# Kernel tuning notes

Hardware: AMD Instinct MI355X
Metric: run time of the kernel (lower is better)

Reference implementation:

```python
import jax, jax.numpy as jnp
import numpy as np
from jax import lax

B, L_IN, D, D_INNER = 4, 1024, 512, 512
H, DK = 8, 64
WIN = [4, 4, 4]
INNER_SIZE = 5   # temporal intra-level neighborhood size
SEM_K = 32       # opt.semantic_node: topk per level for semantic mask
N_LAYER = 2


def _build_temporal_mask(input_size, window_size, inner_size):
    # faithful port of Encoder.get_mask (Pyraformer-Naive mask)
    all_size = [input_size]
    for w in window_size:
        all_size.append(all_size[-1] // w)
    L = sum(all_size)
    m = np.zeros((L, L), dtype=np.float32)
    iw = inner_size // 2
    starts = [sum(all_size[:i]) for i in range(len(all_size))]
    for li, n in enumerate(all_size):
        st = starts[li]
        for i in range(st, st + n):
            m[i, max(i - iw, st):min(i + iw + 1, st + n)] = 1
    for li in range(1, len(all_size)):
        st = starts[li]
        prev = all_size[li - 1]
        w = window_size[li - 1]
        for i in range(st, st + all_size[li]):
            ls = st - prev + (i - st) * w
            rs = st if i == st + all_size[li] - 1 else st - prev + (i - st + 1) * w
            m[i, ls:rs] = 1
            m[ls:rs, i] = 1
    return (1 - m).astype(bool), all_size

TMASK_NP, ALL_SIZE = _build_temporal_mask(L_IN, WIN, INNER_SIZE)
L_TOT = sum(ALL_SIZE)  # 1360


def _ln(x, g, b, eps):
    mu = jnp.mean(x, axis=-1, keepdims=True)
    var = jnp.mean(jnp.square(x - mu), axis=-1, keepdims=True)
    return (x - mu) * lax.rsqrt(var + eps) * g + b


def _mha(x, Wq, Wk, Wv, fcW, fcb, g, b, mask):
    # post-norm MHA (normalize_before=False), dropout disabled (eval)
    Bq, L, _ = x.shape
    q = (x @ Wq).reshape(Bq, L, H, DK)
    k = (x @ Wk).reshape(Bq, L, H, DK)
    v = (x @ Wv).reshape(Bq, L, H, DK)
    a = jnp.einsum('bqhd,bkhd->bhqk', q, k) / np.float32(DK ** 0.5)
    a = jnp.where(mask, -jnp.inf, a)
    p = jax.nn.softmax(a, axis=-1)
    o = jnp.einsum('bhqk,bkhd->bqhd', p, v).reshape(Bq, L, H * DK)
    return _ln(o @ fcW + fcb + x, g, b, 1e-6)


def _semantic_mask(x):
    # get_semantic_mask: per-level cosine similarity, mask topk-most-similar within each level
    nrm = jnp.linalg.norm(x, axis=-1, keepdims=True)
    xn = x / jnp.maximum(nrm, 1e-8)
    sim = jnp.einsum('bid,bjd->bij', xn, xn)
    Bq = x.shape[0]
    mask = jnp.zeros((Bq, L_TOT, L_TOT), dtype=bool)
    bidx = jnp.arange(Bq)[:, None, None]
    start = 0
    for n in ALL_SIZE:
        k = min(n, SEM_K)
        blk = sim[:, start:start + n, start:start + n]
        idx = lax.top_k(blk, k)[1]              # [B, n, k]
        ridx = jnp.arange(n)[None, :, None]
        bm = jnp.zeros((Bq, n, n), dtype=bool).at[bidx, ridx, idx].set(True)
        mask = mask.at[:, start:start + n, start:start + n].set(bm)
        start += n
    return mask


def _bottleneck(x, dW, db, cW, cb, uW, ub, g, b):
    t = jnp.transpose(x @ dW + db, (0, 2, 1))  # [B, d_inner, L]
    outs = []
    for i in range(len(WIN)):
        t = lax.conv_general_dilated(t, cW[i], (WIN[i],), 'VALID',
                                     dimension_numbers=('NCH', 'OIH', 'NCH')) + cb[i][None, :, None]
        t = t / np.float32(np.sqrt(1.0 + 1e-5))  # eval BatchNorm with identity running stats
        t = jax.nn.elu(t)
        outs.append(t)
    pyr = jnp.transpose(jnp.concatenate(outs, axis=2), (0, 2, 1)) @ uW + ub
    return _ln(jnp.concatenate([x, pyr], axis=1), g, b, 1e-5)


def _forward(x_enc, down_W, down_b, conv_W, conv_b, up_W, up_b, bc_ln_g, bc_ln_b,
             attn_Wq, attn_Wk, attn_Wv, attn_fcW, attn_fcb, attn_ln_g, attn_ln_b,
             ffn_W1, ffn_b1, ffn_W2, ffn_b2, ffn_ln_g, ffn_ln_b):
    tmask = jnp.asarray(TMASK_NP)[None, None]  # [1,1,Lt,Lt]
    x = _bottleneck(x_enc, down_W, down_b, conv_W, conv_b, up_W, up_b, bc_ln_g, bc_ln_b)
    for l in range(N_LAYER):
        res = x
        t_out = _mha(x, attn_Wq[l, 0], attn_Wk[l, 0], attn_Wv[l, 0], attn_fcW[l, 0],
                     attn_fcb[l, 0], attn_ln_g[l, 0], attn_ln_b[l, 0], tmask)
        smask = _semantic_mask(x)[:, None]     # [B,1,Lt,Lt]
        s_out = _mha(x, attn_Wq[l, 1], attn_Wk[l, 1], attn_Wv[l, 1], attn_fcW[l, 1],
                     attn_fcb[l, 1], attn_ln_g[l, 1], attn_ln_b[l, 1], smask)
        x = (t_out + s_out + res) / 3.0
        res = x
        h = jax.nn.relu(x @ ffn_W1[l] + ffn_b1[l])
        x = _ln(h @ ffn_W2[l] + ffn_b2[l] + res, ffn_ln_g[l], ffn_ln_b[l], 1e-6)
    return x


def setup_inputs() -> dict:
    key = jax.random.key(0)
    ks = jax.random.split(key, 16)
    s = 0.02
    inp = {
        'x_enc': jax.random.normal(ks[0], (B, L_IN, D), jnp.float32),
        'down_W': jax.random.normal(ks[1], (D, D_INNER), jnp.float32) * s,
        'down_b': jnp.zeros((D_INNER,), jnp.float32),
        'conv_W': jax.random.normal(ks[2], (3, D_INNER, D_INNER, WIN[0]), jnp.float32) * s,
        'conv_b': jnp.zeros((3, D_INNER), jnp.float32),
        'up_W': jax.random.normal(ks[3], (D_INNER, D), jnp.float32) * s,
        'up_b': jnp.zeros((D,), jnp.float32),
        'bc_ln_g': jnp.ones((D,), jnp.float32),
        'bc_ln_b': jnp.zeros((D,), jnp.float32),
        'attn_Wq': jax.random.normal(ks[4], (N_LAYER, 2, D, H * DK), jnp.float32) * s,
        'attn_Wk': jax.random.normal(ks[5], (N_LAYER, 2, D, H * DK), jnp.float32) * s,
        'attn_Wv': jax.random.normal(ks[6], (N_LAYER, 2, D, H * DK), jnp.float32) * s,
        'attn_fcW': jax.random.normal(ks[7], (N_LAYER, 2, H * DK, D), jnp.float32) * s,
        'attn_fcb': jnp.zeros((N_LAYER, 2, D), jnp.float32),
        'attn_ln_g': jnp.ones((N_LAYER, 2, D), jnp.float32),
        'attn_ln_b': jnp.zeros((N_LAYER, 2, D), jnp.float32),
        'ffn_W1': jax.random.normal(ks[8], (N_LAYER, D, D_INNER), jnp.float32) * s,
        'ffn_b1': jnp.zeros((N_LAYER, D_INNER), jnp.float32),
        'ffn_W2': jax.random.normal(ks[9], (N_LAYER, D_INNER, D), jnp.float32) * s,
        'ffn_b2': jnp.zeros((N_LAYER, D), jnp.float32),
        'ffn_ln_g': jnp.ones((N_LAYER, D), jnp.float32),
        'ffn_ln_b': jnp.zeros((N_LAYER, D), jnp.float32),
    }
    return inp


def reference(x_enc, down_W, down_b, conv_W, conv_b, up_W, up_b, bc_ln_g, bc_ln_b,
              attn_Wq, attn_Wk, attn_Wv, attn_fcW, attn_fcb, attn_ln_g, attn_ln_b,
              ffn_W1, ffn_b1, ffn_W2, ffn_b2, ffn_ln_g, ffn_ln_b):
    return _forward(x_enc, down_W, down_b, conv_W, conv_b, up_W, up_b, bc_ln_g, bc_ln_b,
                    attn_Wq, attn_Wk, attn_Wv, attn_fcW, attn_fcb, attn_ln_g, attn_ln_b,
                    ffn_W1, ffn_b1, ffn_W2, ffn_b2, ffn_ln_g, ffn_ln_b)
```

## Files before the change

### kernel.cpp

```cpp
#include <hip/hip_runtime.h>
#include <float.h>
#include <math.h>
#include <stdint.h>

#define LT 1360
#define BB 4
#define DM 512
#define NHH 8
#define NBLE 2785280
#define MBW 24
#define QSCALE 0.18033688f

typedef __attribute__((ext_vector_type(8))) short short8;
typedef __attribute__((ext_vector_type(4))) float f32x4;
typedef unsigned long long u64;

__device__ __forceinline__ ushort f2b(float x){
    uint32_t u = __float_as_uint(x);
    return (ushort)((u + 0x7fffu + ((u >> 16) & 1u)) >> 16);
}
__device__ __forceinline__ float b2f(ushort u){
    return __uint_as_float(((uint32_t)u) << 16);
}
__device__ __forceinline__ float ex2(float x){
    float r;
    asm("v_exp_f32 %0, %1" : "=v"(r) : "v"(x));
    return r;
}
__device__ __forceinline__ uint32_t pkbf(float lo, float hi){
    uint32_t r;
    asm("v_cvt_pk_bf16_f32 %0, %1, %2" : "=v"(r) : "v"(lo), "v"(hi));
    return r;
}

#define SG0 0
#define SG1 1048576
#define SG2 (SG1 + 65536)
#define SG3 (SG2 + 4096)
#define SBT (SG3 + 256)

__device__ __forceinline__ void blk_info(int i, int& bi, int& st, int& n){
    if (i < 1024){ bi = 0; st = 0;    n = 1024; }
    else if (i < 1280){ bi = 1; st = 1024; n = 256; }
    else if (i < 1344){ bi = 2; st = 1280; n = 64; }
    else { bi = 3; st = 1344; n = 16; }
}

__global__ __launch_bounds__(256)
void build_tidx(int* __restrict__ idx, int* __restrict__ cnt){
    int i = blockIdx.x * 256 + threadIdx.x;
    if (i >= LT) return;
    int bi, st, n; blk_info(i, bi, st, n);
    int c = 0; int* row = idx + i * 12;
    int lo = (i - 2 > st) ? i - 2 : st;
    int hi = (i + 2 < st + n - 1) ? i + 2 : st + n - 1;
    for (int j = lo; j <= hi; j++) row[c++] = j;
    if (bi < 3) row[c++] = st + n + (i - st) / 4;
    if (bi > 0){
        int stc = st - n * 4;
        int base = stc + (i - st) * 4;
        for (int t = 0; t < 4; t++) row[c++] = base + t;
    }
    cnt[i] = c;
    for (int t = c; t < 12; t++) row[t] = 0;
}

__global__ __launch_bounds__(256)
void wtrans(const float* __restrict__ W, ushort* __restrict__ Wt, int K, int N, long dstStride){
    int mat = blockIdx.z;
    const float* Ws = W + (size_t)mat * K * N;
    ushort* Wd = Wt + (size_t)mat * dstStride;
    int k0 = blockIdx.y << 6, n0 = blockIdx.x << 6;
    __shared__ ushort t[64][72];
    int tid = threadIdx.x;
    #pragma unroll
    for (int p = 0; p < 4; p++){
        int idx = tid + (p << 8);
        int r = idx >> 4, c4 = (idx & 15) << 2;
        float4 v = *(const float4*)(Ws + (size_t)(k0 + r) * N + n0 + c4);
        t[c4+0][r] = f2b(v.x); t[c4+1][r] = f2b(v.y);
        t[c4+2][r] = f2b(v.z); t[c4+3][r] = f2b(v.w);
    }
    __syncthreads();
    #pragma unroll
    for (int p = 0; p < 4; p++){
        int idx = tid + (p << 8);
        int r = idx >> 4, c4 = (idx & 15) << 2;
        *(uint2*)&Wd[(size_t)(n0 + r) * K + k0 + c4] = *(uint2*)&t[r][c4];
    }
}

__global__ __launch_bounds__(256)
void wconv(const float* __restrict__ cw, ushort* __restrict__ wt){
    int conv = blockIdx.y;
    const float* src = cw + (size_t)conv * 512 * 512 * 4;
    ushort* dst = wt + (size_t)conv * 2048 * 512;
    int idx = blockIdx.x * 256 + threadIdx.x;
    int o = idx >> 11, rest = idx & 2047;
    int k = rest >> 9, ii = rest & 511;
    dst[idx] = f2b(src[((size_t)(o << 9) + ii) * 4 + k]);
}

__global__ __launch_bounds__(256)
void gemm_qkv(const ushort* __restrict__ A, const ushort* __restrict__ Bw,
              void* __restrict__ Cout, int M, int N, int K)
{
    __shared__ ushort As[64][72];
    __shared__ ushort Bs[128][72];
    int tid = threadIdx.x;
    int lane = tid & 63, w = tid >> 6, quad = lane >> 4, l15 = lane & 15;
    int gm = blockIdx.y << 6, gn = blockIdx.x << 7;
    int arow = tid >> 2, ac = (tid & 3) << 4;
    int brow = tid >> 1, bc = (tid & 1) << 5;
    f32x4 acc[4][2];
    #pragma unroll
    for (int mi = 0; mi < 4; mi++)
        #pragma unroll
        for (int ni = 0; ni < 2; ni++)
            acc[mi][ni] = (f32x4){0.f,0.f,0.f,0.f};
    const ushort* Ap = A + (size_t)(gm + arow) * K + ac;
    const ushort* Bp = Bw + (size_t)(gn + brow) * K + bc;
    uint4 a0r = *(const uint4*)(Ap);
    uint4 a1r = *(const uint4*)(Ap + 8);
    uint4 b0r = *(const uint4*)(Bp);
    uint4 b1r = *(const uint4*)(Bp + 8);
    uint4 b2r = *(const uint4*)(Bp + 16);
    uint4 b3r = *(const uint4*)(Bp + 24);
    *(uint4*)&As[arow][ac]     = a0r;  *(uint4*)&As[arow][ac + 8]  = a1r;
    *(uint4*)&Bs[brow][bc]     = b0r;  *(uint4*)&Bs[brow][bc + 8]  = b1r;
    *(uint4*)&Bs[brow][bc + 16] = b2r; *(uint4*)&Bs[brow][bc + 24] = b3r;
    __syncthreads();
    for (int k0 = 0; k0 < K; k0 += 64){
        bool nx = (k0 + 64 < K);
        if (nx){
            a0r = *(const uint4*)(Ap + k0 + 64);
            a1r = *(const uint4*)(Ap + k0 + 72);
            b0r = *(const uint4*)(Bp + k0 + 64);
            b1r = *(const uint4*)(Bp + k0 + 72);
            b2r = *(const uint4*)(Bp + k0 + 80);
            b3r = *(const uint4*)(Bp + k0 + 88);
        }
        __builtin_amdgcn_s_setprio(1);
        #pragma unroll
        for (int kk = 0; kk < 2; kk++){
            short8 af[4], bf[2];
            #pragma unroll
            for (int mi = 0; mi < 4; mi++)
                af[mi] = *(const short8*)&As[(mi << 4) + l15][(kk << 5) + (quad << 3)];
            #pragma unroll
            for (int ni = 0; ni < 2; ni++)
                bf[ni] = *(const short8*)&Bs[(w << 5) + (ni << 4) + l15][(kk << 5) + (quad << 3)];
            #pragma unroll
            for (int mi = 0; mi < 4; mi++)
                #pragma unroll
                for (int ni = 0; ni < 2; ni++)
                    acc[mi][ni] = __builtin_amdgcn_mfma_f32_16x16x32_bf16(af[mi], bf[ni], acc[mi][ni], 0, 0, 0);
        }
        __builtin_amdgcn_s_setprio(0);
        if (nx){
            __syncthreads();
            *(uint4*)&As[arow][ac]     = a0r;  *(uint4*)&As[arow][ac + 8]  = a1r;
            *(uint4*)&Bs[brow][bc]     = b0r;  *(uint4*)&Bs[brow][bc + 8]  = b1r;
            *(uint4*)&Bs[brow][bc + 16] = b2r; *(uint4*)&Bs[brow][bc + 24] = b3r;
            __syncthreads();
        }
    }
    int seg = gn >> 9, gc = gn & 511;
    ushort* Ob = (ushort*)Cout;
    if (seg == 0){
        #pragma unroll
        for (int mi = 0; mi < 4; mi++)
            #pragma unroll
            for (int r = 0; r < 4; r++){
                int row = gm + (mi << 4) + (quad << 2) + r;
                #pragma unroll
                for (int ni = 0; ni < 2; ni++){
                    int c5 = gc + (w << 5) + (ni << 4) + l15;
                    Ob[(size_t)row * 512 + c5] = f2b(acc[mi][ni][r] * QSCALE);
                }
            }
    } else if (seg == 1){
        #pragma unroll
        for (int mi = 0; mi < 4; mi++)
            #pragma unroll
            for (int r = 0; r < 4; r++){
                int row = gm + (mi << 4) + (quad << 2) + r;
                #pragma unroll
                for (int ni = 0; ni < 2; ni++){
                    int c5 = gc + (w << 5) + (ni << 4) + l15;
                    Ob[(size_t)2*NBLE + (size_t)row * 512 + c5] = f2b(acc[mi][ni][r]);
                }
            }
    } else {
        __syncthreads();
        #pragma unroll
        for (int mi = 0; mi < 4; mi++)
            #pragma unroll
            for (int r = 0; r < 4; r++){
                int rloc = (mi << 4) + (quad << 2) + r;
                int row = gm + rloc;
                #pragma unroll
                for (int ni = 0; ni < 2; ni++){
                    int cloc = (w << 5) + (ni << 4) + l15;
                    ushort hv = f2b(acc[mi][ni][r]);
                    Ob[(size_t)5*NBLE + (size_t)row * 512 + gc + cloc] = hv;
                    Bs[cloc][rloc] = hv;
                }
            }
        __syncthreads();
        int colw = tid >> 3;
        int jo = (tid & 7) << 3;
        int rr = gm + jo;
        int bb = rr / LT;
        int ii = rr - bb * LT;
        #pragma unroll
        for (int cc = 0; cc < 4; cc++){
            int c = colw + (cc << 5);
            uint4 tv = *(const uint4*)&Bs[c][jo];
            ushort* dst = Ob + (size_t)4*NBLE + ((size_t)(bb * 512 + gc + c)) * LT + ii;
            *(uint4*)dst = tv;
        }
    }
}

template<int ABF>
__global__ __launch_bounds__(256)
void gemm64t(const void* __restrict__ Avp, const ushort* __restrict__ Bw,
             const float* __restrict__ bias, const float* __restrict__ Rres,
             void* __restrict__ Cout, int M, int N, int K,
             int act, int omode, int mpb, int orpb, int ooff)
{
    __shared__ ushort As[64][72];
    __shared__ ushort Bs[64][72];
    int tid = threadIdx.x;
    int lane = tid & 63, w = tid >> 6, quad = lane >> 4, l15 = lane & 15;
    int gm = blockIdx.y << 6, gn = blockIdx.x << 6;
    int wr = (w >> 1) << 5, wc = (w & 1) << 5;
    int srow = tid >> 2, sc = (tid & 3) << 4;
    f32x4 acc[2][2];
    #pragma unroll
    for (int mi = 0; mi < 2; mi++)
        #pragma unroll
        for (int ni = 0; ni < 2; ni++)
            acc[mi][ni] = (f32x4){0.f,0.f,0.f,0.f};
    const float*  Af = (const float*)Avp;
    const ushort* Ab = (const ushort*)Avp;
    size_t aoff = (size_t)(gm + srow) * K + sc;
    const ushort* Bp = Bw + (size_t)(gn + srow) * K + sc;
    uint4 aR0, aR1, bR0, bR1;
    float4 f0, f1, f2v, f3v;
    if (ABF){
        aR0 = *(const uint4*)(Ab + aoff);
        aR1 = *(const uint4*)(Ab + aoff + 8);
    } else {
        f0  = *(const float4*)(Af + aoff);
        f1  = *(const float4*)(Af + aoff + 4);
        f2v = *(const float4*)(Af + aoff + 8);
        f3v = *(const float4*)(Af + aoff + 12);
    }
    bR0 = *(const uint4*)(Bp);
    bR1 = *(const uint4*)(Bp + 8);
    if (!ABF){
        aR0.x = (uint32_t)f2b(f0.x)  | ((uint32_t)f2b(f0.y)  << 16);
        aR0.y = (uint32_t)f2b(f0.z)  | ((uint32_t)f2b(f0.w)  << 16);
        aR0.z = (uint32_t)f2b(f1.x)  | ((uint32_t)f2b(f1.y)  << 16);
        aR0.w = (uint32_t)f2b(f1.z)  | ((uint32_t)f2b(f1.w)  << 16);
        aR1.x = (uint32_t)f2b(f2v.x) | ((uint32_t)f2b(f2v.y) << 16);
        aR1.y = (uint32_t)f2b(f2v.z) | ((uint32_t)f2b(f2v.w) << 16);
        aR1.z = (uint32_t)f2b(f3v.x) | ((uint32_t)f2b(f3v.y) << 16);
        aR1.w = (uint32_t)f2b(f3v.z) | ((uint32_t)f2b(f3v.w) << 16);
    }
    *(uint4*)&As[srow][sc]     = aR0;
    *(uint4*)&As[srow][sc + 8] = aR1;
    *(uint4*)&Bs[srow][sc]     = bR0;
    *(uint4*)&Bs[srow][sc + 8] = bR1;
    __syncthreads();
    for (int k0 = 0; k0 < K; k0 += 64){
        bool nx = (k0 + 64 < K);
        if (nx){
            if (ABF){
                aR0 = *(const uint4*)(Ab + aoff + k0 + 64);
                aR1 = *(const uint4*)(Ab + aoff + k0 + 72);
            } else {
                f0  = *(const float4*)(Af + aoff + k0 + 64);
                f1  = *(const float4*)(Af + aoff + k0 + 68);
                f2v = *(const float4*)(Af + aoff + k0 + 72);
                f3v = *(const float4*)(Af + aoff + k0 + 76);
            }
            bR0 = *(const uint4*)(Bp + k0 + 64);
            bR1 = *(const uint4*)(Bp + k0 + 72);
        }
        __builtin_amdgcn_s_setprio(1);
        #pragma unroll
        for (int kk = 0; kk < 2; kk++){
            short8 af0 = *(const short8*)&As[wr + l15][(kk << 5) + (quad << 3)];
            short8 af1 = *(const short8*)&As[wr + 16 + l15][(kk << 5) + (quad << 3)];
            short8 bf0 = *(const short8*)&Bs[wc + l15][(kk << 5) + (quad << 3)];
            short8 bf1 = *(const short8*)&Bs[wc + 16 + l15][(kk << 5) + (quad << 3)];
            acc[0][0] = __builtin_amdgcn_mfma_f32_16x16x32_bf16(af0, bf0, acc[0][0], 0, 0, 0);
            acc[0][1] = __builtin_amdgcn_mfma_f32_16x16x32_bf16(af0, bf1, acc[0][1], 0, 0, 0);
            acc[1][0] = __builtin_amdgcn_mfma_f32_16x16x32_bf16(af1, bf0, acc[1][0], 0, 0, 0);
            acc[1][1] = __builtin_amdgcn_mfma_f32_16x16x32_bf16(af1, bf1, acc[1][1], 0, 0, 0);
        }
        __builtin_amdgcn_s_setprio(0);
        if (nx){
            __syncthreads();
            if (!ABF){
                aR0.x = (uint32_t)f2b(f0.x)  | ((uint32_t)f2b(f0.y)  << 16);
                aR0.y = (uint32_t)f2b(f0.z)  | ((uint32_t)f2b(f0.w)  << 16);
                aR0.z = (uint32_t)f2b(f1.x)  | ((uint32_t)f2b(f1.y)  << 16);
                aR0.w = (uint32_t)f2b(f1.z)  | ((uint32_t)f2b(f1.w)  << 16);
                aR1.x = (uint32_t)f2b(f2v.x) | ((uint32_t)f2b(f2v.y) << 16);
                aR1.y = (uint32_t)f2b(f2v.z) | ((uint32_t)f2b(f2v.w) << 16);
                aR1.z = (uint32_t)f2b(f3v.x) | ((uint32_t)f2b(f3v.y) << 16);
                aR1.w = (uint32_t)f2b(f3v.z) | ((uint32_t)f2b(f3v.w) << 16);
            }
            *(uint4*)&As[srow][sc]     = aR0;
            *(uint4*)&As[srow][sc + 8] = aR1;
            *(uint4*)&Bs[srow][sc]     = bR0;
            *(uint4*)&Bs[srow][sc + 8] = bR1;
            __syncthreads();
        }
    }
    #pragma unroll
    for (int mi = 0; mi < 2; mi++){
        #pragma unroll
        for (int r = 0; r < 4; r++){
            int row = gm + wr + (mi << 4) + (quad << 2) + r;
            #pragma unroll
            for (int ni = 0; ni < 2; ni++){
                int col = gn + wc + (ni << 4) + l15;
                float v = acc[mi][ni][r];
                if (bias) v += bias[col];
                if (Rres) v += Rres[(size_t)row * N + col];
                if (act == 2){ v = fmaxf(v, 0.f); }
                if (omode == 0){
                    int orow = mpb ? (row / mpb) * orpb + ooff + (row % mpb) : row;
                    ((float*)Cout)[(size_t)orow * N + col] = v;
                } else {
                    ((ushort*)Cout)[(size_t)row * N + col] = f2b(v);
                }
            }
        }
    }
}

__global__ __launch_bounds__(256)
void gemm_sk(const float* __restrict__ A, const ushort* __restrict__ Bw,
             float* __restrict__ P, int M, int N, int K, int kslice)
{
    __shared__ ushort As[64][40];
    __shared__ ushort Bs[64][40];
    int tid = threadIdx.x;
    int lane = tid & 63, w = tid >> 6, quad = lane >> 4, l15 = lane & 15;
    int gm = blockIdx.y << 6, gn = blockIdx.x << 6;
    int wr = (w >> 1) << 5, wc = (w & 1) << 5;
    int srow = tid >> 2, sc8 = (tid & 3) << 3;
    int ks = blockIdx.z * kslice;
    f32x4 acc[2][2];
    #pragma unroll
    for (int mi = 0; mi < 2; mi++)
        #pragma unroll
        for (int ni = 0; ni < 2; ni++)
            acc[mi][ni] = (f32x4){0.f,0.f,0.f,0.f};
    const float* Ap = A + (size_t)(gm + srow) * K;
    const ushort* Bp = Bw + (size_t)(gn + srow) * K;
    for (int k0 = ks; k0 < ks + kslice; k0 += 32){
        float4 a0 = *(const float4*)(Ap + k0 + sc8);
        float4 a1 = *(const float4*)(Ap + k0 + sc8 + 4);
        uint4 av;
        av.x = (uint32_t)f2b(a0.x) | ((uint32_t)f2b(a0.y) << 16);
        av.y = (uint32_t)f2b(a0.z) | ((uint32_t)f2b(a0.w) << 16);
        av.z = (uint32_t)f2b(a1.x) | ((uint32_t)f2b(a1.y) << 16);
        av.w = (uint32_t)f2b(a1.z) | ((uint32_t)f2b(a1.w) << 16);
        *(uint4*)&As[srow][sc8] = av;
        *(uint4*)&Bs[srow][sc8] = *(const uint4*)(Bp + k0 + sc8);
        __syncthreads();
        short8 af0 = *(const short8*)&As[wr + l15][quad << 3];
        short8 af1 = *(const short8*)&As[wr + 16 + l15][quad << 3];
        short8 bf0 = *(const short8*)&Bs[wc + l15][quad << 3];
        short8 bf1 = *(const short8*)&Bs[wc + 16 + l15][quad << 3];
        acc[0][0] = __builtin_amdgcn_mfma_f32_16x16x32_bf16(af0, bf0, acc[0][0], 0, 0, 0);
        acc[0][1] = __builtin_amdgcn_mfma_f32_16x16x32_bf16(af0, bf1, acc[0][1], 0, 0, 0);
        acc[1][0] = __builtin_amdgcn_mfma_f32_16x16x32_bf16(af1, bf0, acc[1][0], 0, 0, 0);
        acc[1][1] = __builtin_amdgcn_mfma_f32_16x16x32_bf16(af1, bf1, acc[1][1], 0, 0, 0);
        __syncthreads();
    }
    float* Pz = P + (size_t)blockIdx.z * M * N;
    #pragma unroll
    for (int mi = 0; mi < 2; mi++){
        #pragma unroll
        for (int r = 0; r < 4; r++){
            int row = gm + wr + (mi << 4) + (quad << 2) + r;
            #pragma unroll
            for (int ni = 0; ni < 2; ni++){
                int col = gn + wc + (ni << 4) + l15;
                Pz[(size_t)row * N + col] = acc[mi][ni][r];
            }
        }
    }
}

__global__ __launch_bounds__(256)
void sk_reduce(const float* __restrict__ P, const float* __restrict__ bias,
               float* __restrict__ C, int MN, int S)
{
    int idx = (blockIdx.x * 256 + threadIdx.x) << 2;
    if (idx >= MN) return;
    float4 s = {0.f, 0.f, 0.f, 0.f};
    for (int z = 0; z < S; z++){
        float4 v = *(const float4*)(P + (size_t)z * MN + idx);
        s.x += v.x; s.y += v.y; s.z += v.z; s.w += v.w;
    }
    const float cscale = 0.9999950000375f;
    int col = idx & 511;
    float o[4] = {s.x, s.y, s.z, s.w};
    #pragma unroll
    for (int t = 0; t < 4; t++){
        float v = (o[t] + bias[col + t]) * cscale;
        o[t] = (v > 0.f) ? v : expm1f(v);
    }
    *(float4*)(C + idx) = (float4){o[0], o[1], o[2], o[3]};
}

__global__ __launch_bounds__(256)
void sim_mfma(const ushort* __restrict__ XH, const ushort* __restrict__ XL,
              float* __restrict__ SIM){
    __shared__ ushort Ah[64][40], Al[64][40], Bh[64][40], Bl[64][40];
    int x = blockIdx.x, b = blockIdx.y;
    int ti, tj, st, n, goff;
    if (x < 256){ ti = x >> 4; tj = x & 15; st = 0; n = 1024; goff = SG0; }
    else if (x < 272){ int y = x - 256; ti = y >> 2; tj = y & 3; st = 1024; n = 256; goff = SG1; }
    else if (x == 272){ ti = 0; tj = 0; st = 1280; n = 64; goff = SG2; }
    else { ti = 0; tj = 0; st = 1344; n = 16; goff = SG3; }
    const ushort* XbH = XH + (((size_t)b * LT + st) << 9);
    const ushort* XbL = XL + (((size_t)b * LT + st) << 9);
    float* Cb = SIM + (size_t)b * SBT + goff;
    int gm = ti << 6, gn = tj << 6;
    int tid = threadIdx.x;
    int lane = tid & 63, w = tid >> 6, quad = lane >> 4, l15 = lane & 15;
    int wr = (w >> 1) << 5, wc = (w & 1) << 5;
    int srow = tid >> 2, sc8 = (tid & 3) << 3;
    int ra = gm + srow; if (ra > n - 1) ra = n - 1;
    int rb = gn + srow; if (rb > n - 1) rb = n - 1;
    f32x4 acc[2][2];
    #pragma unroll
    for (int mi = 0; mi < 2; mi++)
        #pragma unroll
        for (int ni = 0; ni < 2; ni++)
            acc[mi][ni] = (f32x4){0.f,0.f,0.f,0.f};
    for (int k0 = 0; k0 < 512; k0 += 32){
        *(uint4*)&Ah[srow][sc8] = *(const uint4*)(XbH + ((size_t)ra << 9) + k0 + sc8);
        *(uint4*)&Al[srow][sc8] = *(const uint4*)(XbL + ((size_t)ra << 9) + k0 + sc8);
        *(uint4*)&Bh[srow][sc8] = *(const uint4*)(XbH + ((size_t)rb << 9) + k0 + sc8);
        *(uint4*)&Bl[srow][sc8] = *(const uint4*)(XbL + ((size_t)rb << 9) + k0 + sc8);
        __syncthreads();
        short8 ah0 = *(const short8*)&Ah[wr + l15][quad << 3];
        short8 ah1 = *(const short8*)&Ah[wr + 16 + l15][quad << 3];
        short8 al0 = *(const short8*)&Al[wr + l15][quad << 3];
        short8 al1 = *(const short8*)&Al[wr + 16 + l15][quad << 3];
        short8 bh0 = *(const short8*)&Bh[wc + l15][quad << 3];
        short8 bh1 = *(const short8*)&Bh[wc + 16 + l15][quad << 3];
        short8 bl0 = *(const short8*)&Bl[wc + l15][quad << 3];
        short8 bl1 = *(const short8*)&Bl[wc + 16 + l15][quad << 3];
        acc[0][0] = __builtin_amdgcn_mfma_f32_16x16x32_bf16(ah0, bh0, acc[0][0], 0, 0, 0);
        acc[0][0] = __builtin_amdgcn_mfma_f32_16x16x32_bf16(ah0, bl0, acc[0][0], 0, 0, 0);
        acc[0][0] = __builtin_amdgcn_mfma_f32_16x16x32_bf16(al0, bh0, acc[0][0], 0, 0, 0);
        acc[0][1] = __builtin_amdgcn_mfma_f32_16x16x32_bf16(ah0, bh1, acc[0][1], 0, 0, 0);
        acc[0][1] = __builtin_amdgcn_mfma_f32_16x16x32_bf16(ah0, bl1, acc[0][1], 0, 0, 0);
        acc[0][1] = __builtin_amdgcn_mfma_f32_16x16x32_bf16(al0, bh1, acc[0][1], 0, 0, 0);
        acc[1][0] = __builtin_amdgcn_mfma_f32_16x16x32_bf16(ah1, bh0, acc[1][0], 0, 0, 0);
        acc[1][0] = __builtin_amdgcn_mfma_f32_16x16x32_bf16(ah1, bl0, acc[1][0], 0, 0, 0);
        acc[1][0] = __builtin_amdgcn_mfma_f32_16x16x32_bf16(al1, bh0, acc[1][0], 0, 0, 0);
        acc[1][1] = __builtin_amdgcn_mfma_f32_16x16x32_bf16(ah1, bh1, acc[1][1], 0, 0, 0);
        acc[1][1] = __builtin_amdgcn_mfma_f32_16x16x32_bf16(ah1, bl1, acc[1][1], 0, 0, 0);
        acc[1][1] = __builtin_amdgcn_mfma_f32_16x16x32_bf16(al1, bh1, acc[1][1], 0, 0, 0);
        __syncthreads();
    }
    #pragma unroll
    for (int mi = 0; mi < 2; mi++){
        #pragma unroll
        for (int r = 0; r < 4; r++){
            int row = gm + wr + (mi << 4) + (quad << 2) + r;
            if (row < n){
                #pragma unroll
                for (int ni = 0; ni < 2; ni++){
                    int col = gn + wc + (ni << 4) + l15;
                    if (col < n) Cb[(size_t)row * n + col] = acc[mi][ni][r];
                }
            }
        }
    }
}

__global__ __launch_bounds__(256)
void pcat_copy(const float* __restrict__ C1, const float* __restrict__ C2,
               const float* __restrict__ C3, float* __restrict__ PC){
    int idx = blockIdx.x * 256 + threadIdx.x;
    int d = idx & 511;
    int r = (idx >> 9) % 336;
    int b = idx / (336 * 512);
    float v;
    if (r < 256)       v = C1[(((size_t)b * 256 + r) << 9) + d];
    else if (r < 320)  v = C2[(((size_t)b * 64 + (r - 256)) << 9) + d];
    else               v = C3[(((size_t)b * 16 + (r - 320)) << 9) + d];
    PC[idx] = v;
}

__global__ __launch_bounds__(256)
void xenc_copy(const float* __restrict__ xe, float* __restrict__ dst){
    int idx = blockIdx.x * 256 + threadIdx.x;
    int d = idx & 511;
    int l = (idx >> 9) & 1023;
    int b = idx >> 19;
    dst[(((size_t)b * LT + l) << 9) + d] = xe[idx];
}

__global__ __launch_bounds__(256)
void ln_kernel(const float* __restrict__ in, const float* __restrict__ g,
               const float* __restrict__ bta, float* __restrict__ out,
               ushort* __restrict__ ob, float eps){
    int wid = threadIdx.x >> 6, lane = threadIdx.x & 63;
    int row = blockIdx.x * 4 + wid;
    const float* p = in + ((size_t)row << 9);
    float vals[8]; float s = 0.f, s2 = 0.f;
    #pragma unroll
    for (int t = 0; t < 8; t++){
        float v = p[lane + t * 64]; vals[t] = v; s += v; s2 += v * v;
    }
    #pragma unroll
    for (int off = 32; off; off >>= 1){
        s  += __shfl_xor(s,  off, 64);
        s2 += __shfl_xor(s2, off, 64);
    }
    float mu = s * (1.f / 512.f);
    float var = s2 * (1.f / 512.f) - mu * mu;
    float r = rsqrtf(var + eps);
    float* q = out + ((size_t)row << 9);
    ushort* qb = ob ? ob + ((size_t)row << 9) : nullptr;
    #pragma unroll
    for (int t = 0; t < 8; t++){
        int c = lane + t * 64;
        float v = (vals[t] - mu) * r * g[c] + bta[c];
        q[c] = v;
        if (qb) qb[c] = f2b(v);
    }
}

__global__ __launch_bounds__(256)
void ln_add3(const float* __restrict__ in, const float* __restrict__ g,
             const float* __restrict__ bta, const float* __restrict__ T,
             float* __restrict__ X, ushort* __restrict__ ob, float eps){
    int wid = threadIdx.x >> 6, lane = threadIdx.x & 63;
    int row = blockIdx.x * 4 + wid;
    const float* p = in + ((size_t)row << 9);
    float vals[8]; float s = 0.f, s2 = 0.f;
    #pragma unroll
    for (int t = 0; t < 8; t++){
        float v = p[lane + t * 64]; vals[t] = v; s += v; s2 += v * v;
    }
    #pragma unroll
    for (int off = 32; off; off >>= 1){
        s  += __shfl_xor(s,  off, 64);
        s2 += __shfl_xor(s2, off, 64);
    }
    float mu = s * (1.f / 512.f);
    float var = s2 * (1.f / 512.f) - mu * mu;
    float r = rsqrtf(var + eps);
    const float* tp = T + ((size_t)row << 9);
    float* xp = X + ((size_t)row << 9);
    ushort* qb = ob + ((size_t)row << 9);
    #pragma unroll
    for (int t = 0; t < 8; t++){
        int c = lane + t * 64;
        float sn = (vals[t] - mu) * r * g[c] + bta[c];
        float nv = (tp[c] + sn + xp[c]) * (1.f / 3.f);
        xp[c] = nv;
        qb[c] = f2b(nv);
    }
}

__global__ __launch_bounds__(256)
void rownorm_kernel(const float* __restrict__ in, ushort* __restrict__ XHp,
                    ushort* __restrict__ XLp){
    int wid = threadIdx.x >> 6, lane = threadIdx.x & 63;
    int row = blockIdx.x * 4 + wid;
    const float* p = in + ((size_t)row << 9);
    float vals[8]; float s2 = 0.f;
    #pragma unroll
    for (int t = 0; t < 8; t++){
        float v = p[lane + t * 64]; vals[t] = v; s2 += v * v;
    }
    #pragma unroll
    for (int off = 32; off; off >>= 1) s2 += __shfl_xor(s2, off, 64);
    float inv = 1.f / fmaxf(sqrtf(s2), 1e-8f);
    ushort* qh = XHp + ((size_t)row << 9);
    ushort* ql = XLp + ((size_t)row << 9);
    #pragma unroll
    for (int t = 0; t < 8; t++){
        float v = vals[t] * inv;
        ushort h = f2b(v);
        qh[lane + t * 64] = h;
        ql[lane + t * 64] = f2b(v - b2f(h));
    }
}

__global__ __launch_bounds__(256)
void topk_sel(const float* __restrict__ SIM, u64* __restrict__ MB){
    int wid = threadIdx.x >> 6, lane = threadIdx.x & 63;
    int r = blockIdx.x * 4 + wid;
    int b = r / LT, i = r % LT;
    int bi, st, n; blk_info(i, bi, st, n);
    u64* mrow = MB + ((size_t)b * LT + i) * MBW;
    if (n == 16){
        u64 myw = 0;
        if (lane == 21) myw = ~0ULL;
        if (lane < MBW) mrow[lane] = myw;
        return;
    }
    int goff = (bi == 0) ? SG0 : (bi == 1) ? SG1 : SG2;
    const float* srow = SIM + (size_t)b * SBT + goff + (size_t)(i - st) * n;
    int ns = n >> 6;
    float vals[16];
    #pragma unroll
    for (int t = 0; t < 16; t++)
        vals[t] = (t < ns) ? srow[lane + (t << 6)] : -FLT_MAX;

    float c[32];
    #pragma unroll
    for (int t = 0; t < 16; t++) c[t] = vals[t];
    #pragma unroll
    for (int k = 2; k <= 16; k <<= 1){
        #pragma unroll
        for (int j = k >> 1; j > 0; j >>= 1){
            #pragma unroll
            for (int t = 0; t < 16; t++){
                int l = t ^ j;
                if (l > t){
                    float lo = fminf(c[t], c[l]);
                    float hi = fmaxf(c[t], c[l]);
                    if ((t & k) == 0){ c[t] = hi; c[l] = lo; }
                    else             { c[t] = lo; c[l] = hi; }
                }
            }
        }
    }
    #pragma unroll
    for (int t = 16; t < 32; t++) c[t] = -FLT_MAX;

    float V32;
    #pragma unroll
    for (int rd = 0; rd < 6; rd++){
        float f[32];
        #pragma unroll
        for (int t = 0; t < 32; t++) f[t] = __shfl_xor(c[t], 1 << rd, 64);
        float m[32];
        #pragma unroll
        for (int t = 0; t < 32; t++) m[t] = fmaxf(c[t], f[31 - t]);
        if (rd < 5){
            #pragma unroll
            for (int d = 16; d >= 1; d >>= 1){
                #pragma unroll
                for (int t = 0; t < 32; t++){
                    if ((t & d) == 0){
                        float lo = fminf(m[t], m[t + d]);
                        m[t] = fmaxf(m[t], m[t + d]);
                        m[t + d] = lo;
                    }
                }
            }
            #pragma unroll
            for (int t = 0; t < 32; t++) c[t] = m[t];
        } else {
            float mn = m[0];
            #pragma unroll
            for (int t = 1; t < 32; t++) mn = fminf(mn, m[t]);
            V32 = mn;
        }
    }

    int cnt_gt = 0;
    #pragma unroll
    for (int t = 0; t < 16; t++){
        u64 bg = __ballot(vals[t] > V32);
        cnt_gt += __popcll(bg);
    }
    int need = 32 - cnt_gt;
    u64 lmask = (1ULL << lane) - 1;
    u64 myw = 0;
    if (lane == 21) myw = 0xFFFFFFFFFFFF0000ULL;
    int eqrun = 0;
    int w0 = st >> 6;
    #pragma unroll
    for (int t = 0; t < 16; t++){
        bool eq = (vals[t] == V32);
        u64 beq = __ballot(eq);
        int below = __popcll(beq & lmask);
        bool sel = (vals[t] > V32) || (eq && (eqrun + below) < need);
        eqrun += __popcll(beq);
        u64 wsel = __ballot(sel);
        if (t < ns && lane == w0 + t) myw = wsel;
    }
    if (lane < MBW) mrow[lane] = myw;
}

__global__ __launch_bounds__(256)
void attn_sparse(const ushort* __restrict__ Q, const ushort* __restrict__ Kp,
                 const ushort* __restrict__ Vn, const int* __restrict__ IDX,
                 const int* __restrict__ CNT, ushort* __restrict__ O){
    int wid = threadIdx.x >> 6, lane = threadIdx.x & 63;
    int row = blockIdx.x * 4 + wid;
    int b = row / (NHH * LT);
    int rem = row % (NHH * LT);
    int h = rem / LT, i = rem % LT;
    int c = CNT[i];
    int jl = IDX[i * 12 + (lane % 12)];
    float qd = b2f(Q[(((size_t)b * LT + i) << 9) + h * 64 + lane]);
    const ushort* kb = Kp + (((size_t)b * LT) << 9) + h * 64 + lane;
    const ushort* vb = Vn + (((size_t)b * LT) << 9) + h * 64 + lane;
    int jj[12];
    #pragma unroll
    for (int t = 0; t < 12; t++) jj[t] = __shfl(jl, t, 64);
    float kv[12], vv[12];
    #pragma unroll
    for (int t = 0; t < 12; t++){
        kv[t] = b2f(kb[(size_t)jj[t] << 9]);
        vv[t] = b2f(vb[(size_t)jj[t] << 9]);
    }
    float lsum = 0.f, o = 0.f;
    #pragma unroll
    for (int t = 0; t < 12; t++){
        float s = qd * kv[t];
        #pragma unroll
        for (int off = 32; off; off >>= 1) s += __shfl_xor(s, off, 64);
        float p = (t < c) ? exp2f(s) : 0.f;
        lsum += p;
        o += p * vv[t];
    }
    O[(((size_t)b * LT + i) << 9) + h * 64 + lane] = f2b(o / lsum);
}

__global__ __launch_bounds__(256)
void flash_mfma(const ushort* __restrict__ Q, const ushort* __restrict__ Kp,
                const ushort* __restrict__ Vt, const u64* __restrict__ MB,
                float* __restrict__ FO0, float* __restrict__ FO1,
                float* __restrict__ LP)
{
    __shared__ ushort Ks[64][76];
    __shared__ ushort Vs[64][76];
    __shared__ ushort Ps[4][16][76];
    int bh = blockIdx.x, b = bh >> 3, h = bh & 7;
    int q0 = blockIdx.y << 6;
    int half = blockIdx.z;
    int tid = threadIdx.x;
    int w = tid >> 6, lane = tid & 63, quad = lane >> 4, l15 = lane & 15;

    int qm = q0 + w * 16 + l15;
    int qmc = (qm < LT) ? qm : (LT - 1);
    const ushort* qp = Q + ((size_t)(b * LT + qmc) << 9) + h * 64 + (quad << 3);
    short8 qf0 = *(const short8*)qp;
    short8 qf1 = *(const short8*)(qp + 32);

    float l_acc[4] = {0.f, 0.f, 0.f, 0.f};
    f32x4 Oacc[4];
    #pragma unroll
    for (int dt = 0; dt < 4; dt++) Oacc[dt] = (f32x4){0.f,0.f,0.f,0.f};

    int srow = tid >> 2, sc = (tid & 3) << 4;
    int ktS = half * 11, ktE = ktS + 11;

    const ushort* kpp = Kp + ((size_t)(b * LT + (ktS << 6) + srow) << 9) + h * 64 + sc;
    const ushort* vpp = Vt + (size_t)(b * 512 + h * 64 + srow) * LT + (ktS << 6) + sc;
    int mr0 = q0 + (w << 4) + (quad << 2);
    const u64* mpp = MB + ((size_t)b * LT + mr0) * MBW + ktS;

    {
        uint4 k0v = *(const uint4*)kpp;
        uint4 k1v = *(const uint4*)(kpp + 8);
        uint4 v0v = *(const uint4*)vpp;
        uint4 v1v = *(const uint4*)(vpp + 8);
        kpp += 64 * 512; vpp += 64;
        *(uint4*)&Ks[srow][sc]     = k0v;
        *(uint4*)&Ks[srow][sc + 8] = k1v;
        *(uint4*)&Vs[srow][sc]     = v0v;
        *(uint4*)&Vs[srow][sc + 8] = v1v;
    }
    __syncthreads();

    for (int kt = ktS; kt < ktE; kt++){
        bool havenext = (kt + 1 < ktE);
        uint4 kn0, kn1, vn0, vn1;
        if (havenext){
            kn0 = *(const uint4*)kpp;
            kn1 = *(const uint4*)(kpp + 8);
            vn0 = *(const uint4*)vpp;
            vn1 = *(const uint4*)(vpp + 8);
            kpp += 64 * 512; vpp += 64;
        }
        u64 mb0 = mpp[0], mb1 = mpp[MBW], mb2 = mpp[2 * MBW], mb3 = mpp[3 * MBW];
        mpp++;
        f32x4 s[4];
        #pragma unroll
        for (int nt = 0; nt < 4; nt++) s[nt] = (f32x4){0.f,0.f,0.f,0.f};
        __builtin_amdgcn_s_setprio(1);
        #pragma unroll
        for (int nt = 0; nt < 4; nt++){
            short8 kf0 = *(const short8*)&Ks[(nt << 4) + l15][quad << 3];
            short8 kf1 = *(const short8*)&Ks[(nt << 4) + l15][32 + (quad << 3)];
            s[nt] = __builtin_amdgcn_mfma_f32_16x16x32_bf16(qf0, kf0, s[nt], 0, 0, 0);
            s[nt] = __builtin_amdgcn_mfma_f32_16x16x32_bf16(qf1, kf1, s[nt], 0, 0, 0);
        }
        __builtin_amdgcn_s_setprio(0);
        u64 mbs[4] = {mb0, mb1, mb2, mb3};
        #pragma unroll
        for (int r = 0; r < 4; r++){
            u64 sh = mbs[r] >> l15;
            uint32_t blo = (uint32_t)sh, bhi = (uint32_t)(sh >> 32);
            float p0 = (blo & 1u)         ? 0.f : ex2(s[0][r]);
            float p1 = ((blo >> 16) & 1u) ? 0.f : ex2(s[1][r]);
            float p2 = (bhi & 1u)         ? 0.f : ex2(s[2][r]);
            float p3 = ((bhi >> 16) & 1u) ? 0.f : ex2(s[3][r]);
            uint32_t pk01 = pkbf(p0, p1);
            uint32_t pk23 = pkbf(p2, p3);
            int prow = (quad << 2) + r;
            Ps[w][prow][l15]      = (ushort)pk01;
            Ps[w][prow][16 + l15] = (ushort)(pk01 >> 16);
            Ps[w][prow][32 + l15] = (ushort)pk23;
            Ps[w][prow][48 + l15] = (ushort)(pk23 >> 16);
            l_acc[r] += (p0 + p1) + (p2 + p3);
        }
        short8 pf0 = *(const short8*)&Ps[w][l15][quad << 3];
        short8 pf1 = *(const short8*)&Ps[w][l15][32 + (quad << 3)];
        __builtin_amdgcn_s_setprio(1);
        #pragma unroll
        for (int dt = 0; dt < 4; dt++){
            short8 vf0 = *(const short8*)&Vs[(dt << 4) + l15][quad << 3];
            short8 vf1 = *(const short8*)&Vs[(dt << 4) + l15][32 + (quad << 3)];
            Oacc[dt] = __builtin_amdgcn_mfma_f32_16x16x32_bf16(pf0, vf0, Oacc[dt], 0, 0, 0);
            Oacc[dt] = __builtin_amdgcn_mfma_f32_16x16x32_bf16(pf1, vf1, Oacc[dt], 0, 0, 0);
        }
        __builtin_amdgcn_s_setprio(0);
        if (havenext){
            __syncthreads();
            *(uint4*)&Ks[srow][sc]     = kn0;
            *(uint4*)&Ks[srow][sc + 8] = kn1;
            *(uint4*)&Vs[srow][sc]     = vn0;
            *(uint4*)&Vs[srow][sc + 8] = vn1;
            __syncthreads();
        }
    }
    #pragma unroll
    for (int r = 0; r < 4; r++){
        #pragma unroll
        for (int off = 1; off < 16; off <<= 1)
            l_acc[r] += __shfl_xor(l_acc[r], off, 64);
    }
    float* FO = half ? FO1 : FO0;
    float* Lp = LP + (size_t)half * BB * NHH * LT;
    #pragma unroll
    for (int r = 0; r < 4; r++){
        int qrow = q0 + (w << 4) + (quad << 2) + r;
        if (qrow < LT){
            #pragma unroll
            for (int dt = 0; dt < 4; dt++)
                FO[((size_t)(b * LT + qrow) << 9) + h * 64 + (dt << 4) + l15] = Oacc[dt][r];
            if (l15 == 0)
                Lp[(size_t)(b * NHH + h) * LT + qrow] = l_acc[r];
        }
    }
}

__global__ __launch_bounds__(256)
void flash_combine(const float* __restrict__ FO0, const float* __restrict__ FO1,
                   const float* __restrict__ LP, ushort* __restrict__ AO){
    int wid = threadIdx.x >> 6, lane = threadIdx.x & 63;
    int row = blockIdx.x * 4 + wid;
    int b = row / LT, q = row % LT;
    size_t base = (size_t)row << 9;
    const float* Lp0 = LP;
    const float* Lp1 = LP + (size_t)BB * NHH * LT;
    #pragma unroll
    for (int t = 0; t < 8; t++){
        size_t li = (size_t)(b * NHH + t) * LT + q;
        float inv = 1.f / (Lp0[li] + Lp1[li]);
        int c = lane + t * 64;
        AO[base + c] = f2b((FO0[base + c] + FO1[base + c]) * inv);
    }
}

extern "C" void kernel_launch(void* const* d_in, const int* in_sizes, int n_in,
                              void* d_out, int out_size, void* d_ws, size_t ws_size,
                              hipStream_t stream)
{
    const float* x_enc   = (const float*)d_in[0];
    const float* down_W  = (const float*)d_in[1];
    const float* down_b  = (const float*)d_in[2];
    const float* conv_W  = (const float*)d_in[3];
    const float* conv_b  = (const float*)d_in[4];
    const float* up_W    = (const float*)d_in[5];
    const float* up_b    = (const float*)d_in[6];
    const float* bc_g    = (const float*)d_in[7];
    const float* bc_b    = (const float*)d_in[8];
    const float* aWq     = (const float*)d_in[9];
    const float* aWk     = (const float*)d_in[10];
    const float* aWv     = (const float*)d_in[11];
    const float* afcW    = (const float*)d_in[12];
    const float* afcb    = (const float*)d_in[13];
    const float* alng    = (const float*)d_in[14];
    const float* alnb    = (const float*)d_in[15];
    const float* fW1     = (const float*)d_in[16];
    const float* fb1     = (const float*)d_in[17];
    const float* fW2     = (const float*)d_in[18];
    const float* fb2     = (const float*)d_in[19];
    const float* flng    = (const float*)d_in[20];
    const float* flnb    = (const float*)d_in[21];

    const size_t NBL = (size_t)NBLE;
    float* X   = (float*)d_ws;
    float* TMP = X   + NBL;
    float* Qb  = TMP + NBL;
    float* Kb  = Qb  + NBL;
    float* Vb  = Kb  + NBL;
    float* AO  = Vb  + NBL;
    float* TO  = AO  + NBL;
    float* SO  = TO  + NBL;
    u64* MBm = (u64*)(SO + NBL);
    int* TIDX = (int*)(MBm + (size_t)BB * LT * MBW);
    int* TCNT = TIDX + (size_t)LT * 12;
    ushort* WG = (ushort*)(TCNT + LT);
    const size_t M512 = 262144;
    ushort* WdownT = WG;                 size_t wo = M512;
    ushort* WupT   = WG + wo;            wo += M512;
    ushort* Wqkv   = WG + wo;            wo += 12 * M512;
    ushort* WfT    = WG + wo;            wo += 4 * M512;
    ushort* W1T    = WG + wo;            wo += 2 * M512;
    ushort* W2T    = WG + wo;            wo += 2 * M512;
    ushort* WCt    = WG + wo;            wo += 3 * 1048576;
    float* LP = (float*)(WG + wo);
    size_t need = 8 * NBL * sizeof(float) + (size_t)BB * LT * MBW * 8
                + (size_t)LT * 13 * 4 + wo * sizeof(ushort)
                + (size_t)2 * BB * NHH * LT * 4;
    if (ws_size < need) return;

    float* Y    = Qb;
    float* C1   = Kb;
    float* C2   = C1 + (size_t)BB*256*512;
    float* C3   = C2 + (size_t)BB*64*512;
    float* PCAT = Vb;
    float* SKP  = AO;
    ushort* XNh = (ushort*)AO;
    ushort* XNl = XNh + NBLE;
    float* SIMB = Qb;
    ushort* QbH = (ushort*)Qb;
    ushort* KbH = (ushort*)Kb;
    ushort* VtH = (ushort*)Vb;
    ushort* VnH = VtH + NBLE;
    float* FO0  = TMP;
    float* FO1  = SO;
    ushort* XB  = (ushort*)SO;
    ushort* AOb = (ushort*)AO;
    ushort* HfB = (ushort*)Qb;

    auto gemmN = [&](const void* A, int abf, const ushort* Bw, const float* bias,
                     const float* res, void* C, int M,
                     int act, int omode, int mpb, int orpb, int ooff){
        dim3 grid(8, M / 64);
        if (abf) gemm64t<1><<<grid, 256, 0, stream>>>(A, Bw, bias, res, C, M, 512, 512,
                                                      act, omode, mpb, orpb, ooff);
        else     gemm64t<0><<<grid, 256, 0, stream>>>(A, Bw, bias, res, C, M, 512, 512,
                                                      act, omode, mpb, orpb, ooff);
    };
    auto convG = [&](const float* A, const ushort* Bw, const float* bias,
                     float* C, int M){
        const int S = 8, K = 2048, N = 512;
        gemm_sk<<<dim3(8, M / 64, S), 256, 0, stream>>>(A, Bw, SKP, M, N, K, K / S);
        sk_reduce<<<(M * N) / 1024, 256, 0, stream>>>(SKP, bias, C, M * N, S);
    };

    build_tidx<<<(LT + 255) / 256, 256, 0, stream>>>(TIDX, TCNT);
    wtrans<<<dim3(8, 8, 1), 256, 0, stream>>>(down_W, WdownT, 512, 512, M512);
    wtrans<<<dim3(8, 8, 1), 256, 0, stream>>>(up_W,   WupT,   512, 512, M512);
    wtrans<<<dim3(8, 8, 4), 256, 0, stream>>>(aWq,  Wqkv + 0 * M512, 512, 512, 3 * (long)M512);
    wtrans<<<dim3(8, 8, 4), 256, 0, stream>>>(aWk,  Wqkv + 1 * M512, 512, 512, 3 * (long)M512);
    wtrans<<<dim3(8, 8, 4), 256, 0, stream>>>(aWv,  Wqkv + 2 * M512, 512, 512, 3 * (long)M512);
    wtrans<<<dim3(8, 8, 4), 256, 0, stream>>>(afcW, WfT, 512, 512, M512);
    wtrans<<<dim3(8, 8, 2), 256, 0, stream>>>(fW1,  W1T, 512, 512, M512);
    wtrans<<<dim3(8, 8, 2), 256, 0, stream>>>(fW2,  W2T, 512, 512, M512);
    wconv<<<dim3(4096, 3), 256, 0, stream>>>(conv_W, WCt);

    gemmN(x_enc, 0, WdownT, down_b, nullptr, Y, BB*1024, 0, 0, 0, 0, 0);
    convG(Y,  WCt,             conv_b + 0,    C1, BB*256);
    convG(C1, WCt + 1048576,   conv_b + 512,  C2, BB*64);
    convG(C2, WCt + 2*1048576, conv_b + 1024, C3, BB*16);
    pcat_copy<<<(BB*336*512)/256, 256, 0, stream>>>(C1, C2, C3, PCAT);
    gemmN(PCAT, 0, WupT, up_b, nullptr, TMP, BB*336, 0, 0, 336, LT, 1024);
    xenc_copy<<<(BB*1024*512)/256, 256, 0, stream>>>(x_enc, TMP);
    ln_kernel<<<(BB*LT)/4, 256, 0, stream>>>(TMP, bc_g, bc_b, X, XB, 1e-5f);

    for (int l = 0; l < 2; l++){
        rownorm_kernel<<<(BB*LT)/4, 256, 0, stream>>>(X, XNh, XNl);
        sim_mfma<<<dim3(274, BB), 256, 0, stream>>>(XNh, XNl, SIMB);
        topk_sel<<<(BB*LT)/4, 256, 0, stream>>>(SIMB, MBm);

        for (int j = 0; j < 2; j++){
            int li = l * 2 + j;
            const float* bf = afcb + (size_t)li * 512;
            const float* lg = alng + (size_t)li * 512;
            const float* lb = alnb + (size_t)li * 512;
            gemm_qkv<<<dim3(12, 85), 256, 0, stream>>>(XB, Wqkv + (size_t)li * 3 * M512,
                                                       QbH, BB*LT, 1536, 512);
            if (j == 0){
                attn_sparse<<<(BB*NHH*LT)/4, 256, 0, stream>>>(QbH, KbH, VnH, TIDX, TCNT, AOb);
            } else {
                flash_mfma<<<dim3(32, 22, 2), 256, 0, stream>>>(QbH, KbH, VtH, MBm, FO0, FO1, LP);
                flash_combine<<<(BB*LT)/4, 256, 0, stream>>>(FO0, FO1, LP, AOb);
            }
            gemmN(AOb, 1, WfT + (size_t)li * M512, bf, X, TMP, BB*LT, 0, 0, 0, 0, 0);
            if (j == 0)
                ln_kernel<<<(BB*LT)/4, 256, 0, stream>>>(TMP, lg, lb, TO, nullptr, 1e-6f);
            else
                ln_add3<<<(BB*LT)/4, 256, 0, stream>>>(TMP, lg, lb, TO, X, XB, 1e-6f);
        }

        gemmN(XB,  1, W1T + (size_t)l * M512, fb1 + (size_t)l*512, nullptr, HfB, BB*LT, 2, 1, 0, 0, 0);
        gemmN(HfB, 1, W2T + (size_t)l * M512, fb2 + (size_t)l*512, X, TMP, BB*LT, 0, 0, 0, 0, 0);
        ln_kernel<<<(BB*LT)/4, 256, 0, stream>>>(TMP, flng + (size_t)l*512, flnb + (size_t)l*512,
                                                 (l == 1) ? (float*)d_out : X,
                                                 (l == 1) ? nullptr : XB, 1e-6f);
    }
}
```

Baseline: 821.5 us.

## Drop split-K flash attention and combine kernel; double-buffer K/V tiles in LDS

The flash attention kernel no longer splits the 22 key tiles across two blocks. One block now covers all keys, normalizes by the softmax sum and writes bf16 output directly, so the float partial outputs and the separate combine kernel go away. K/V tiles are double-buffered in shared memory, which cuts the two barriers per iteration to one. The trade-off is half as many blocks (704), which lowers parallelism on a large GPU, and more LDS per block.

```diff
diff --git a/kernel.cpp b/kernel.cpp
--- a/kernel.cpp
+++ b/kernel.cpp
@@ -743,15 +743,13 @@
 __global__ __launch_bounds__(256)
 void flash_mfma(const ushort* __restrict__ Q, const ushort* __restrict__ Kp,
                 const ushort* __restrict__ Vt, const u64* __restrict__ MB,
-                float* __restrict__ FO0, float* __restrict__ FO1,
-                float* __restrict__ LP)
+                ushort* __restrict__ AO)
 {
-    __shared__ ushort Ks[64][76];
-    __shared__ ushort Vs[64][76];
+    __shared__ ushort Ks[2][64][76];
+    __shared__ ushort Vs[2][64][76];
     __shared__ ushort Ps[4][16][76];
     int bh = blockIdx.x, b = bh >> 3, h = bh & 7;
     int q0 = blockIdx.y << 6;
-    int half = blockIdx.z;
     int tid = threadIdx.x;
     int w = tid >> 6, lane = tid & 63, quad = lane >> 4, l15 = lane & 15;
 
@@ -767,12 +765,11 @@
     for (int dt = 0; dt < 4; dt++) Oacc[dt] = (f32x4){0.f,0.f,0.f,0.f};
 
     int srow = tid >> 2, sc = (tid & 3) << 4;
-    int ktS = half * 11, ktE = ktS + 11;
-
-    const ushort* kpp = Kp + ((size_t)(b * LT + (ktS << 6) + srow) << 9) + h * 64 + sc;
-    const ushort* vpp = Vt + (size_t)(b * 512 + h * 64 + srow) * LT + (ktS << 6) + sc;
+
+    const ushort* kpp = Kp + ((size_t)(b * LT + srow) << 9) + h * 64 + sc;
+    const ushort* vpp = Vt + (size_t)(b * 512 + h * 64 + srow) * LT + sc;
     int mr0 = q0 + (w << 4) + (quad << 2);
-    const u64* mpp = MB + ((size_t)b * LT + mr0) * MBW + ktS;
+    const u64* mpp = MB + ((size_t)b * LT + mr0) * MBW;
 
     {
         uint4 k0v = *(const uint4*)kpp;
@@ -780,15 +777,16 @@
         uint4 v0v = *(const uint4*)vpp;
         uint4 v1v = *(const uint4*)(vpp + 8);
         kpp += 64 * 512; vpp += 64;
-        *(uint4*)&Ks[srow][sc]     = k0v;
-        *(uint4*)&Ks[srow][sc + 8] = k1v;
-        *(uint4*)&Vs[srow][sc]     = v0v;
-        *(uint4*)&Vs[srow][sc + 8] = v1v;
+        *(uint4*)&Ks[0][srow][sc]     = k0v;
+        *(uint4*)&Ks[0][srow][sc + 8] = k1v;
+        *(uint4*)&Vs[0][srow][sc]     = v0v;
+        *(uint4*)&Vs[0][srow][sc + 8] = v1v;
     }
     __syncthreads();
 
-    for (int kt = ktS; kt < ktE; kt++){
-        bool havenext = (kt + 1 < ktE);
+    for (int kt = 0; kt < 22; kt++){
+        int cur = kt & 1;
+        bool havenext = (kt + 1 < 22);
         uint4 kn0, kn1, vn0, vn1;
         if (havenext){
             kn0 = *(const uint4*)kpp;
@@ -805,8 +803,8 @@
         __builtin_amdgcn_s_setprio(1);
         #pragma unroll
         for (int nt = 0; nt < 4; nt++){
-            short8 kf0 = *(const short8*)&Ks[(nt << 4) + l15][quad << 3];
-            short8 kf1 = *(const short8*)&Ks[(nt << 4) + l15][32 + (quad << 3)];
+            short8 kf0 = *(const short8*)&Ks[cur][(nt << 4) + l15][quad << 3];
+            short8 kf1 = *(const short8*)&Ks[cur][(nt << 4) + l15][32 + (quad << 3)];
             s[nt] = __builtin_amdgcn_mfma_f32_16x16x32_bf16(qf0, kf0, s[nt], 0, 0, 0);
             s[nt] = __builtin_amdgcn_mfma_f32_16x16x32_bf16(qf1, kf1, s[nt], 0, 0, 0);
         }
@@ -834,20 +832,20 @@
         __builtin_amdgcn_s_setprio(1);
         #pragma unroll
         for (int dt = 0; dt < 4; dt++){
-            short8 vf0 = *(const short8*)&Vs[(dt << 4) + l15][quad << 3];
-            short8 vf1 = *(const short8*)&Vs[(dt << 4) + l15][32 + (quad << 3)];
+            short8 vf0 = *(const short8*)&Vs[cur][(dt << 4) + l15][quad << 3];
+            short8 vf1 = *(const short8*)&Vs[cur][(dt << 4) + l15][32 + (quad << 3)];
             Oacc[dt] = __builtin_amdgcn_mfma_f32_16x16x32_bf16(pf0, vf0, Oacc[dt], 0, 0, 0);
             Oacc[dt] = __builtin_amdgcn_mfma_f32_16x16x32_bf16(pf1, vf1, Oacc[dt], 0, 0, 0);
         }
         __builtin_amdgcn_s_setprio(0);
         if (havenext){
-            __syncthreads();
-            *(uint4*)&Ks[srow][sc]     = kn0;
-            *(uint4*)&Ks[srow][sc + 8] = kn1;
-            *(uint4*)&Vs[srow][sc]     = vn0;
-            *(uint4*)&Vs[srow][sc + 8] = vn1;
-            __syncthreads();
-        }
+            int nb = cur ^ 1;
+            *(uint4*)&Ks[nb][srow][sc]     = kn0;
+            *(uint4*)&Ks[nb][srow][sc + 8] = kn1;
+            *(uint4*)&Vs[nb][srow][sc]     = vn0;
+            *(uint4*)&Vs[nb][srow][sc + 8] = vn1;
+        }
+        __syncthreads();
     }
     #pragma unroll
     for (int r = 0; r < 4; r++){
@@ -855,36 +853,16 @@
         for (int off = 1; off < 16; off <<= 1)
             l_acc[r] += __shfl_xor(l_acc[r], off, 64);
     }
-    float* FO = half ? FO1 : FO0;
-    float* Lp = LP + (size_t)half * BB * NHH * LT;
     #pragma unroll
     for (int r = 0; r < 4; r++){
         int qrow = q0 + (w << 4) + (quad << 2) + r;
         if (qrow < LT){
+            float inv = 1.f / l_acc[r];
             #pragma unroll
             for (int dt = 0; dt < 4; dt++)
-                FO[((size_t)(b * LT + qrow) << 9) + h * 64 + (dt << 4) + l15] = Oacc[dt][r];
-            if (l15 == 0)
-                Lp[(size_t)(b * NHH + h) * LT + qrow] = l_acc[r];
-        }
-    }
-}
-
-__global__ __launch_bounds__(256)
-void flash_combine(const float* __restrict__ FO0, const float* __restrict__ FO1,
-                   const float* __restrict__ LP, ushort* __restrict__ AO){
-    int wid = threadIdx.x >> 6, lane = threadIdx.x & 63;
-    int row = blockIdx.x * 4 + wid;
-    int b = row / LT, q = row % LT;
-    size_t base = (size_t)row << 9;
-    const float* Lp0 = LP;
-    const float* Lp1 = LP + (size_t)BB * NHH * LT;
-    #pragma unroll
-    for (int t = 0; t < 8; t++){
-        size_t li = (size_t)(b * NHH + t) * LT + q;
-        float inv = 1.f / (Lp0[li] + Lp1[li]);
-        int c = lane + t * 64;
-        AO[base + c] = f2b((FO0[base + c] + FO1[base + c]) * inv);
+                AO[((size_t)(b * LT + qrow) << 9) + h * 64 + (dt << 4) + l15] =
+                    f2b(Oacc[dt][r] * inv);
+        }
     }
 }
 
@@ -937,6 +915,7 @@
     ushort* W2T    = WG + wo;            wo += 2 * M512;
     ushort* WCt    = WG + wo;            wo += 3 * 1048576;
     float* LP = (float*)(WG + wo);
+    (void)LP;
     size_t need = 8 * NBL * sizeof(float) + (size_t)BB * LT * MBW * 8
                 + (size_t)LT * 13 * 4 + wo * sizeof(ushort)
                 + (size_t)2 * BB * NHH * LT * 4;
@@ -955,8 +934,6 @@
     ushort* KbH = (ushort*)Kb;
     ushort* VtH = (ushort*)Vb;
     ushort* VnH = VtH + NBLE;
-    float* FO0  = TMP;
-    float* FO1  = SO;
     ushort* XB  = (ushort*)SO;
     ushort* AOb = (ushort*)AO;
     ushort* HfB = (ushort*)Qb;
@@ -1012,8 +989,7 @@
             if (j == 0){
                 attn_sparse<<<(BB*NHH*LT)/4, 256, 0, stream>>>(QbH, KbH, VnH, TIDX, TCNT, AOb);
             } else {
-                flash_mfma<<<dim3(32, 22, 2), 256, 0, stream>>>(QbH, KbH, VtH, MBm, FO0, FO1, LP);
-                flash_combine<<<(BB*LT)/4, 256, 0, stream>>>(FO0, FO1, LP, AOb);
+                flash_mfma<<<dim3(32, 22), 256, 0, stream>>>(QbH, KbH, VtH, MBm, AOb);
             }
             gemmN(AOb, 1, WfT + (size_t)li * M512, bf, X, TMP, BB*LT, 0, 0, 0, 0, 0);
             if (j == 0)
```

Measured after the change: 806.0 us. No clear change (-1.9%).
